# Kernel tuning notes

Hardware: AMD Instinct MI355X
Metric: run time of the kernel (lower is better)

## Reference

```python
import jax, jax.numpy as jnp
import numpy as np
from jax import lax

N, IN_CH, FEAT, OUT_CH, H, W = 8, 3, 64, 3, 256, 256
EPS = 1e-8


def lrelu(x):
    return jnp.where(x >= 0, x, 0.2 * x)


def conv2d(x, w, b, stride, pad):
    y = lax.conv_general_dilated(x, w, (stride, stride), [(pad, pad), (pad, pad)],
                                 dimension_numbers=('NCHW', 'OIHW', 'NCHW'))
    return y + b[None, :, None, None]


def make_blur_kernel():
    # _make_kernel([1,3,3,1]): outer product, normalized
    k = jnp.array([1.0, 3.0, 3.0, 1.0], jnp.float32)
    k = k[None, :] * k[:, None]
    return k / k.sum()


def blur(x, kernel, pad):
    # upfirdn2d with up=down=1: pad then FIR-convolve (true convolution -> flip kernel)
    n, c, h, w = x.shape
    k = jnp.flip(kernel, (0, 1))[None, None]  # [1,1,kh,kw]
    y = lax.conv_general_dilated(x.reshape(n * c, 1, h, w), k, (1, 1),
                                 [(pad[0], pad[1]), (pad[0], pad[1])],
                                 dimension_numbers=('NCHW', 'OIHW', 'NCHW'))
    return y.reshape(n, c, y.shape[-2], y.shape[-1])


def mod_conv(x, s, w, swW, swb, sbW, sbb, mode, blur_k, activate=True):
    # x [n,c,h,w]; s [n,feat]; w [out,c,k,k]; style 1x1 convs on [n,feat,1,1] == matmuls
    kk = w.shape[-1]
    sw = lrelu(s @ swW.T + swb)                    # [n, c]  (style_weight)
    sb = lrelu(s @ sbW.T + sbb)                    # [n, out] (style_bias)
    weight = w[None] * sw[:, None, :, None, None]  # [n,out,c,k,k]
    d = lax.rsqrt(jnp.sum(weight * weight, axis=(2, 3, 4)) + EPS)
    weight = weight * d[:, :, None, None, None]    # demodulate
    if mode == 'up':
        # conv_transpose2d(stride=2, pad=0) == conv with lhs_dilation=2, pad k-1, flipped kernel
        wf = jnp.flip(weight, (-2, -1))
        def f(xi, wi):
            return lax.conv_general_dilated(xi[None], wi, (1, 1),
                    [(kk - 1, kk - 1)] * 2, lhs_dilation=(2, 2),
                    dimension_numbers=('NCHW', 'OIHW', 'NCHW'))[0]
        y = jax.vmap(f)(x, wf)
        y = blur(y, blur_k * 4.0, (1, 1))          # Blur(pad=(1,1), upsample_factor=2)
    elif mode == 'down':
        xb = blur(x, blur_k, (2, 2))               # Blur(pad=(2,2))
        def f(xi, wi):
            return lax.conv_general_dilated(xi[None], wi, (2, 2), [(0, 0)] * 2,
                    dimension_numbers=('NCHW', 'OIHW', 'NCHW'))[0]
        y = jax.vmap(f)(xb, weight)
    else:
        p = kk // 2
        def f(xi, wi):
            return lax.conv_general_dilated(xi[None], wi, (1, 1), [(p, p)] * 2,
                    dimension_numbers=('NCHW', 'OIHW', 'NCHW'))[0]
        y = jax.vmap(f)(x, weight)
    y = y + sb[:, :, None, None]
    return lrelu(y) if activate else y


def da_forward(x, ref, g0_w, g0_b, gr_w, gr_b,
               c0_w, c0_swW, c0_swb, c0_sbW, c0_sbb,
               mid_w, mid_swW, mid_swb, mid_sbW, mid_sbb,
               c6_w, c6_swW, c6_swb, c6_sbW, c6_sbb):
    bk = make_blur_kernel()
    # guide_net: conv s1/lrelu, conv s2/lrelu, conv s1/lrelu, conv s2/lrelu, conv s1, avgpool(1)
    h = lrelu(conv2d(ref, g0_w, g0_b, 1, 1))
    strides = (2, 1, 2, 1)
    for i in range(4):
        h = conv2d(h, gr_w[i], gr_b[i], strides[i], 1)
        if i < 3:
            h = lrelu(h)
    s = jnp.mean(h, axis=(2, 3))  # [n, feat]; AdaptiveAvgPool2d(1)

    mids = lambda i: (mid_w[i], mid_swW[i], mid_swb[i], mid_sbW[i], mid_sbb[i])
    f0 = mod_conv(x, s, c0_w, c0_swW, c0_swb, c0_sbW, c0_sbb, 'none', bk)
    f1 = mod_conv(f0, s, *mids(0), 'down', bk)
    f1 = mod_conv(f1, s, *mids(1), 'none', bk)
    f2 = mod_conv(f1, s, *mids(2), 'down', bk)
    f2 = mod_conv(f2, s, *mids(3), 'none', bk)
    f3 = mod_conv(f2, s, *mids(4), 'none', bk)
    f3 = mod_conv(f3, s, *mids(5), 'none', bk)
    f4 = mod_conv(f3 + f2, s, *mids(6), 'up', bk)
    f4 = mod_conv(f4, s, *mids(7), 'none', bk)
    f5 = mod_conv(f4 + f1, s, *mids(8), 'up', bk)
    f5 = mod_conv(f5, s, *mids(9), 'none', bk)
    out = mod_conv(f5 + f0, s, c6_w, c6_swW, c6_swb, c6_sbW, c6_sbb, 'none', bk, activate=False)
    return out


def setup_inputs() -> dict:
    key = jax.random.key(0)
    ks = jax.random.split(key, 24)
    f = FEAT
    inv = 1.0 / np.sqrt(f)
    d = {
        'x':   jax.random.normal(ks[0], (N, IN_CH, H, W), jnp.float32),
        'ref': jax.random.normal(ks[1], (N, IN_CH, H, W), jnp.float32),
        'g0_w': jax.random.normal(ks[2], (f, IN_CH, 3, 3), jnp.float32) * (1.0 / np.sqrt(IN_CH * 9)),
        'g0_b': jnp.zeros((f,), jnp.float32),
        'gr_w': jax.random.normal(ks[3], (4, f, f, 3, 3), jnp.float32) * (1.0 / np.sqrt(f * 9)),
        'gr_b': jnp.zeros((4, f), jnp.float32),
        'c0_w':   jax.random.normal(ks[4], (f, IN_CH, 3, 3), jnp.float32),
        'c0_swW': jax.random.normal(ks[5], (IN_CH, f), jnp.float32) * inv,
        'c0_swb': jnp.zeros((IN_CH,), jnp.float32),
        'c0_sbW': jax.random.normal(ks[6], (f, f), jnp.float32) * inv,
        'c0_sbb': jnp.zeros((f,), jnp.float32),
        'mid_w':   jax.random.normal(ks[7], (10, f, f, 3, 3), jnp.float32),
        'mid_swW': jax.random.normal(ks[8], (10, f, f), jnp.float32) * inv,
        'mid_swb': jnp.zeros((10, f), jnp.float32),
        'mid_sbW': jax.random.normal(ks[9], (10, f, f), jnp.float32) * inv,
        'mid_sbb': jnp.zeros((10, f), jnp.float32),
        'c6_w':   jax.random.normal(ks[10], (OUT_CH, f, 3, 3), jnp.float32),
        'c6_swW': jax.random.normal(ks[11], (f, f), jnp.float32) * inv,
        'c6_swb': jnp.zeros((f,), jnp.float32),
        'c6_sbW': jax.random.normal(ks[12], (OUT_CH, f), jnp.float32) * inv,
        'c6_sbb': jnp.zeros((OUT_CH,), jnp.float32),
    }
    return d


def reference(x, ref, g0_w, g0_b, gr_w, gr_b,
              c0_w, c0_swW, c0_swb, c0_sbW, c0_sbb,
              mid_w, mid_swW, mid_swb, mid_sbW, mid_sbb,
              c6_w, c6_swW, c6_swb, c6_sbW, c6_sbb):
    return da_forward(x, ref, g0_w, g0_b, gr_w, gr_b,
                      c0_w, c0_swW, c0_swb, c0_sbW, c0_sbb,
                      mid_w, mid_swW, mid_swb, mid_sbW, mid_sbb,
                      c6_w, c6_swW, c6_swb, c6_sbW, c6_sbb)
```

## Files before the change

### kernel.cpp

```cpp
#include <hip/hip_runtime.h>

#define LRELU(v) ((v) >= 0.f ? (v) : 0.2f * (v))

template<int S>
__global__ void conv64_gemm(const float* __restrict__ in, const float* __restrict__ Wt,
                            const float* __restrict__ bias, float* __restrict__ out,
                            int Hin, int Win, int Hout, int Wout, int pad, int act, int tilesX,
                            long long inStr, long long wStr, long long bStr, long long outStr)
{
    constexpr int CC  = (S == 1) ? 8 : 4;
    constexpr int TIN = (S == 1) ? 18 : 33;
    constexpr int RS  = (S == 1) ? 20 : 36;
    constexpr int NF4 = (S == 1) ? 3 : 5;
    constexpr int PW  = NF4 * 4;
    extern __shared__ float lds[];
    float* it = lds;
    float* wl = lds + CC * TIN * RS;

    int s = blockIdx.y;
    in   += (size_t)s * inStr;
    Wt   += (size_t)s * wStr;
    bias += (size_t)s * bStr;
    out  += (size_t)s * outStr;

    int b  = blockIdx.x;
    int tx = b % tilesX, ty = b / tilesX;
    int t  = threadIdx.x;
    int og = t >> 5;
    int pg = t & 31;
    int r  = pg >> 1, ch = pg & 1;

    float acc[8][8];
    #pragma unroll
    for (int i = 0; i < 8; ++i)
        #pragma unroll
        for (int j = 0; j < 8; ++j) acc[i][j] = 0.f;

    const int y0 = ty * 16 * S - pad;
    const int x0 = tx * 16 * S - pad;
    const size_t plane = (size_t)Hin * Win;

    for (int c0 = 0; c0 < 64; c0 += CC) {
        __syncthreads();
        {
            const float4* src = (const float4*)(Wt + c0 * 9 * 64);
            float4* dst = (float4*)wl;
            for (int i = t; i < CC * 9 * 16; i += 256) dst[i] = src[i];
        }
        for (int rowi = t; rowi < CC * TIN; rowi += 256) {
            int cc = rowi / TIN, rr = rowi - cc * TIN;
            int iy = y0 + rr;
            float* dst = it + (size_t)rowi * RS;
            const float* srow = in + (size_t)(c0 + cc) * plane + (size_t)iy * Win + x0;
            if ((unsigned)iy < (unsigned)Hin && x0 >= 0 && x0 + RS <= Win) {
                #pragma unroll
                for (int q = 0; q < RS / 4; ++q)
                    ((float4*)dst)[q] = ((const float4*)srow)[q];
            } else {
                for (int cl = 0; cl < TIN; ++cl) {
                    int ix = x0 + cl;
                    float v = 0.f;
                    if ((unsigned)iy < (unsigned)Hin && (unsigned)ix < (unsigned)Win)
                        v = in[(size_t)(c0 + cc) * plane + (size_t)iy * Win + ix];
                    dst[cl] = v;
                }
            }
        }
        __syncthreads();
        for (int cc = 0; cc < CC; ++cc) {
            const float* base = it + cc * TIN * RS;
            #pragma unroll
            for (int ky = 0; ky < 3; ++ky) {
                float p[PW];
                const float* rowp = base + (r * S + ky) * RS + ch * 8 * S;
                #pragma unroll
                for (int q = 0; q < NF4; ++q) {
                    float4 f = *(const float4*)(rowp + q * 4);
                    p[q*4+0] = f.x; p[q*4+1] = f.y; p[q*4+2] = f.z; p[q*4+3] = f.w;
                }
                #pragma unroll
                for (int kx = 0; kx < 3; ++kx) {
                    const float* wp = wl + ((cc * 9) + ky * 3 + kx) * 64 + og * 8;
                    float4 wa = *(const float4*)wp;
                    float4 wb = *(const float4*)(wp + 4);
                    float w8[8] = {wa.x, wa.y, wa.z, wa.w, wb.x, wb.y, wb.z, wb.w};
                    #pragma unroll
                    for (int oi = 0; oi < 8; ++oi)
                        #pragma unroll
                        for (int j = 0; j < 8; ++j)
                            acc[oi][j] += w8[oi] * p[j * S + kx];
                }
            }
        }
    }

    int y  = ty * 16 + r;
    int xb = tx * 16 + ch * 8;
    #pragma unroll
    for (int oi = 0; oi < 8; ++oi) {
        int o = og * 8 + oi;
        float bo = bias[o];
        float v[8];
        #pragma unroll
        for (int j = 0; j < 8; ++j) {
            float a = acc[oi][j] + bo;
            v[j] = act ? LRELU(a) : a;
        }
        float* op = out + ((size_t)o * Hout + y) * Wout + xb;
        *(float4*)op       = make_float4(v[0], v[1], v[2], v[3]);
        *(float4*)(op + 4) = make_float4(v[4], v[5], v[6], v[7]);
    }
}

__global__ void conv64_gemm8(const float* __restrict__ in, const float* __restrict__ Wt,
                             const float* __restrict__ bias, float* __restrict__ out,
                             int H, int W, int act, int tilesX,
                             long long inStr, long long wStr, long long bStr, long long outStr)
{
    constexpr int CC = 8, TIN = 10, RS = 12;
    __shared__ float it[CC * TIN * RS];
    __shared__ float wl[CC * 9 * 64];
    int s = blockIdx.y;
    in   += (size_t)s * inStr;
    Wt   += (size_t)s * wStr;
    bias += (size_t)s * bStr;
    out  += (size_t)s * outStr;

    int b  = blockIdx.x;
    int tx = b % tilesX, ty = b / tilesX;
    int t  = threadIdx.x;
    int og = t >> 5, pg = t & 31;
    int r  = pg >> 2, ch = pg & 3;

    float acc[8][2];
    #pragma unroll
    for (int i = 0; i < 8; ++i) { acc[i][0] = 0.f; acc[i][1] = 0.f; }

    const int y0 = ty * 8 - 1, x0 = tx * 8 - 1;
    const size_t plane = (size_t)H * W;

    for (int c0 = 0; c0 < 64; c0 += CC) {
        __syncthreads();
        {
            const float4* src = (const float4*)(Wt + c0 * 9 * 64);
            float4* dst = (float4*)wl;
            for (int i = t; i < CC * 9 * 16; i += 256) dst[i] = src[i];
        }
        for (int rowi = t; rowi < CC * TIN; rowi += 256) {
            int cc = rowi / TIN, rr = rowi - cc * TIN;
            int iy = y0 + rr;
            float* dst = it + rowi * RS;
            const float* srow = in + (size_t)(c0 + cc) * plane + (size_t)iy * W + x0;
            if ((unsigned)iy < (unsigned)H && x0 >= 0 && x0 + RS <= W) {
                #pragma unroll
                for (int q = 0; q < 3; ++q)
                    ((float4*)dst)[q] = ((const float4*)srow)[q];
            } else {
                for (int cl = 0; cl < RS; ++cl) {
                    int ix = x0 + cl;
                    float v = 0.f;
                    if (cl < TIN && (unsigned)iy < (unsigned)H && (unsigned)ix < (unsigned)W)
                        v = in[(size_t)(c0 + cc) * plane + (size_t)iy * W + ix];
                    dst[cl] = v;
                }
            }
        }
        __syncthreads();
        for (int cc = 0; cc < CC; ++cc) {
            const float* base = it + cc * TIN * RS;
            #pragma unroll
            for (int ky = 0; ky < 3; ++ky) {
                const float* rowp = base + (r + ky) * RS + ch * 2;
                float p[4] = {rowp[0], rowp[1], rowp[2], rowp[3]};
                #pragma unroll
                for (int kx = 0; kx < 3; ++kx) {
                    const float* wp = wl + ((cc * 9) + ky * 3 + kx) * 64 + og * 8;
                    float4 wa = *(const float4*)wp;
                    float4 wb = *(const float4*)(wp + 4);
                    float w8[8] = {wa.x, wa.y, wa.z, wa.w, wb.x, wb.y, wb.z, wb.w};
                    #pragma unroll
                    for (int oi = 0; oi < 8; ++oi) {
                        acc[oi][0] += w8[oi] * p[kx];
                        acc[oi][1] += w8[oi] * p[kx + 1];
                    }
                }
            }
        }
    }

    int y = ty * 8 + r, xb = tx * 8 + ch * 2;
    #pragma unroll
    for (int oi = 0; oi < 8; ++oi) {
        int o = og * 8 + oi;
        float bo = bias[o];
        float a0 = acc[oi][0] + bo, a1 = acc[oi][1] + bo;
        if (act) { a0 = LRELU(a0); a1 = LRELU(a1); }
        *(float2*)(out + ((size_t)o * H + y) * W + xb) = make_float2(a0, a1);
    }
}

__global__ void conv3_gemm(const float* __restrict__ in, const float* __restrict__ Wt,
                           const float* __restrict__ bias, float* __restrict__ out,
                           int H, int W, int tilesX,
                           long long inStr, long long wStr, long long bStr, long long outStr)
{
    constexpr int TIN = 18, RS = 20;
    __shared__ float it[3 * TIN * RS];
    __shared__ float wl[27 * 64];
    int s = blockIdx.y;
    in   += (size_t)s * inStr;
    Wt   += (size_t)s * wStr;
    bias += (size_t)s * bStr;
    out  += (size_t)s * outStr;

    int b  = blockIdx.x;
    int tx = b % tilesX, ty = b / tilesX;
    int t  = threadIdx.x;
    {
        const float4* src = (const float4*)Wt;
        float4* dst = (float4*)wl;
        for (int i = t; i < 27 * 16; i += 256) dst[i] = src[i];
    }
    const int y0 = ty * 16 - 1, x0 = tx * 16 - 1;
    const size_t plane = (size_t)H * W;
    for (int rowi = t; rowi < 3 * TIN; rowi += 256) {
        int cc = rowi / TIN, rr = rowi - cc * TIN;
        int iy = y0 + rr;
        float* dst = it + (size_t)rowi * RS;
        const float* srow = in + (size_t)cc * plane + (size_t)iy * W + x0;
        if ((unsigned)iy < (unsigned)H && x0 >= 0 && x0 + RS <= W) {
            #pragma unroll
            for (int q = 0; q < RS / 4; ++q)
                ((float4*)dst)[q] = ((const float4*)srow)[q];
        } else {
            for (int cl = 0; cl < TIN; ++cl) {
                int ix = x0 + cl;
                float v = 0.f;
                if ((unsigned)iy < (unsigned)H && (unsigned)ix < (unsigned)W)
                    v = in[(size_t)cc * plane + (size_t)iy * W + ix];
                dst[cl] = v;
            }
        }
    }
    __syncthreads();

    int og = t >> 5, pg = t & 31;
    int r  = pg >> 1, ch = pg & 1;
    float acc[8][8];
    #pragma unroll
    for (int i = 0; i < 8; ++i)
        #pragma unroll
        for (int j = 0; j < 8; ++j) acc[i][j] = 0.f;

    for (int c = 0; c < 3; ++c) {
        const float* base = it + c * TIN * RS;
        #pragma unroll
        for (int ky = 0; ky < 3; ++ky) {
            float p[12];
            const float* rowp = base + (r + ky) * RS + ch * 8;
            #pragma unroll
            for (int q = 0; q < 3; ++q) {
                float4 f = *(const float4*)(rowp + q * 4);
                p[q*4+0] = f.x; p[q*4+1] = f.y; p[q*4+2] = f.z; p[q*4+3] = f.w;
            }
            #pragma unroll
            for (int kx = 0; kx < 3; ++kx) {
                const float* wp = wl + ((c * 9) + ky * 3 + kx) * 64 + og * 8;
                float4 wa = *(const float4*)wp;
                float4 wb = *(const float4*)(wp + 4);
                float w8[8] = {wa.x, wa.y, wa.z, wa.w, wb.x, wb.y, wb.z, wb.w};
                #pragma unroll
                for (int oi = 0; oi < 8; ++oi)
                    #pragma unroll
                    for (int j = 0; j < 8; ++j)
                        acc[oi][j] += w8[oi] * p[j + kx];
            }
        }
    }

    int y  = ty * 16 + r;
    int xb = tx * 16 + ch * 8;
    #pragma unroll
    for (int oi = 0; oi < 8; ++oi) {
        int o = og * 8 + oi;
        float bo = bias[o];
        float v[8];
        #pragma unroll
        for (int j = 0; j < 8; ++j) {
            float a = acc[oi][j] + bo;
            v[j] = LRELU(a);
        }
        float* op = out + ((size_t)o * H + y) * W + xb;
        *(float4*)op       = make_float4(v[0], v[1], v[2], v[3]);
        *(float4*)(op + 4) = make_float4(v[4], v[5], v[6], v[7]);
    }
}

__global__ void conv64to3_gemm(const float* __restrict__ in, const float* __restrict__ in2,
                               const float* __restrict__ Wt, const float* __restrict__ sb,
                               float* __restrict__ out, int H, int W, int tilesX,
                               long long inStr, long long wStr, long long sbStr, long long outStr)
{
    constexpr int CC = 8, TIN = 18, RS = 20;
    __shared__ float it[CC * TIN * RS];
    __shared__ float wl[CC * 9 * 3];
    int s = blockIdx.y;
    in  += (size_t)s * inStr;
    in2 += (size_t)s * inStr;
    Wt  += (size_t)s * wStr;
    sb  += (size_t)s * sbStr;
    out += (size_t)s * outStr;

    int b  = blockIdx.x;
    int tx = b % tilesX, ty = b / tilesX;
    int t  = threadIdx.x;
    int r  = t >> 4, cl = t & 15;
    const int y0 = ty * 16 - 1, x0 = tx * 16 - 1;
    const size_t plane = (size_t)H * W;

    float acc[3] = {0.f, 0.f, 0.f};

    for (int c0 = 0; c0 < 64; c0 += CC) {
        __syncthreads();
        for (int i = t; i < CC * 9 * 3; i += 256) wl[i] = Wt[c0 * 27 + i];
        for (int rowi = t; rowi < CC * TIN; rowi += 256) {
            int cc = rowi / TIN, rr = rowi - cc * TIN;
            int iy = y0 + rr;
            float* dst = it + (size_t)rowi * RS;
            size_t roff = (size_t)(c0 + cc) * plane + (size_t)iy * W + x0;
            if ((unsigned)iy < (unsigned)H && x0 >= 0 && x0 + RS <= W) {
                #pragma unroll
                for (int q = 0; q < RS / 4; ++q) {
                    float4 a = ((const float4*)(in  + roff))[q];
                    float4 bb = ((const float4*)(in2 + roff))[q];
                    ((float4*)dst)[q] = make_float4(a.x + bb.x, a.y + bb.y, a.z + bb.z, a.w + bb.w);
                }
            } else {
                for (int c2 = 0; c2 < TIN; ++c2) {
                    int ix = x0 + c2;
                    float v = 0.f;
                    if ((unsigned)iy < (unsigned)H && (unsigned)ix < (unsigned)W) {
                        size_t off = (size_t)(c0 + cc) * plane + (size_t)iy * W + ix;
                        v = in[off] + in2[off];
                    }
                    dst[c2] = v;
                }
            }
        }
        __syncthreads();
        for (int cc = 0; cc < CC; ++cc) {
            const float* base = it + cc * TIN * RS;
            #pragma unroll
            for (int ky = 0; ky < 3; ++ky) {
                const float* rowp = base + (r + ky) * RS + cl;
                float p0 = rowp[0], p1 = rowp[1], p2 = rowp[2];
                const float* wr = wl + (cc * 9 + ky * 3) * 3;
                #pragma unroll
                for (int o = 0; o < 3; ++o)
                    acc[o] += wr[o] * p0 + wr[3 + o] * p1 + wr[6 + o] * p2;
            }
        }
    }

    int y = ty * 16 + r, x = tx * 16 + cl;
    #pragma unroll
    for (int o = 0; o < 3; ++o)
        out[((size_t)o * H + y) * W + x] = acc[o] + sb[o];
}

__global__ void upconv64_gemm(const float* __restrict__ in, const float* __restrict__ in2,
                              const float* __restrict__ G2, const float* __restrict__ sb,
                              float* __restrict__ out, int Hin, int Win, int tilesX,
                              long long bufStr, long long sbStr, long long outStr)
{
    constexpr int CC = 4;
    constexpr int RS = 12;
    constexpr int PSTR = 68;
    extern __shared__ float lds[];
    float* it = lds;
    float* wl = lds + CC * 10 * RS;

    int s = blockIdx.y;
    in  += (size_t)s * bufStr;
    in2 += (size_t)s * bufStr;
    G2  += (size_t)s * bufStr;
    sb  += (size_t)s * sbStr;
    out += (size_t)s * outStr;

    int b  = blockIdx.x;
    int tx = b % tilesX, ty = b / tilesX;
    int t  = threadIdx.x;
    int og    = t & 7;
    int pxb   = (t >> 3) & 1;
    int rhalf = (t >> 4) & 7;
    int rpar  = t >> 7;
    int r = 2 * rhalf + rpar;
    const int Y0 = ty * 16, X0 = tx * 16;
    const int gy0 = Y0 / 2 - 1;
    const int gx0 = X0 / 2 - 1;
    const size_t plane = (size_t)Hin * Win;

    float acc[8][8];
    #pragma unroll
    for (int i = 0; i < 8; ++i)
        #pragma unroll
        for (int j = 0; j < 8; ++j) acc[i][j] = 0.f;

    for (int c0 = 0; c0 < 64; c0 += CC) {
        __syncthreads();
        {
            const float4* src = (const float4*)(G2 + (size_t)c0 * 2304);
            for (int i = t; i < CC * 36 * 16; i += 256) {
                int row = i >> 4, q = i & 15;
                ((float4*)(wl + row * PSTR))[q] = src[i];
            }
        }
        for (int rowi = t; rowi < CC * 10; rowi += 256) {
            int cc = rowi / 10, rr = rowi - cc * 10;
            int gi = gy0 + rr;
            float* dst = it + (size_t)rowi * RS;
            size_t roff = (size_t)(c0 + cc) * plane + (size_t)gi * Win + gx0;
            if ((unsigned)gi < (unsigned)Hin && gx0 >= 0 && gx0 + RS <= Win) {
                #pragma unroll
                for (int qq = 0; qq < 3; ++qq) {
                    float4 a = ((const float4*)(in  + roff))[qq];
                    float4 bb = ((const float4*)(in2 + roff))[qq];
                    ((float4*)dst)[qq] = make_float4(a.x + bb.x, a.y + bb.y, a.z + bb.z, a.w + bb.w);
                }
            } else {
                for (int cl = 0; cl < RS; ++cl) {
                    int gj = gx0 + cl;
                    float v = 0.f;
                    if (cl < 10 && (unsigned)gi < (unsigned)Hin && (unsigned)gj < (unsigned)Win) {
                        size_t off = (size_t)(c0 + cc) * plane + (size_t)gi * Win + gj;
                        v = in[off] + in2[off];
                    }
                    dst[cl] = v;
                }
            }
        }
        __syncthreads();
        for (int cc = 0; cc < CC; ++cc) {
            const float* ib = it + cc * 10 * RS;
            const float* wcb = wl + cc * (36 * PSTR) + (rpar * 2 + pxb) * PSTR;
            #pragma unroll
            for (int ty2 = 0; ty2 < 3; ++ty2) {
                float p[12];
                const float* rowp = ib + (rhalf + ty2) * RS;
                #pragma unroll
                for (int qq = 0; qq < 3; ++qq) {
                    float4 f = *(const float4*)(rowp + qq * 4);
                    p[qq*4+0] = f.x; p[qq*4+1] = f.y; p[qq*4+2] = f.z; p[qq*4+3] = f.w;
                }
                #pragma unroll
                for (int tx2 = 0; tx2 < 3; ++tx2) {
                    const float* wp = wcb + (ty2 * 3 + tx2) * (4 * PSTR) + og * 8;
                    float4 wa = *(const float4*)wp;
                    float4 wv = *(const float4*)(wp + 4);
                    float w8[8] = {wa.x, wa.y, wa.z, wa.w, wv.x, wv.y, wv.z, wv.w};
                    #pragma unroll
                    for (int oi = 0; oi < 8; ++oi)
                        #pragma unroll
                        for (int k = 0; k < 8; ++k)
                            acc[oi][k] += w8[oi] * p[k + tx2];
                }
            }
        }
    }

    const int Hout = 2 * Hin, Wout = 2 * Win;
    int y = Y0 + r;
    #pragma unroll
    for (int oi = 0; oi < 8; ++oi) {
        int o = og * 8 + oi;
        float bo = sb[o];
        float v[8];
        #pragma unroll
        for (int k = 0; k < 8; ++k) {
            float a = acc[oi][k] + bo;
            v[k] = LRELU(a);
        }
        float rcv[4];
        #pragma unroll
        for (int j = 0; j < 4; ++j) {
            float snd = pxb ? v[j] : v[4 + j];
            rcv[j] = __shfl_xor(snd, 8, 64);
        }
        float w0 = pxb ? rcv[0] : v[0];
        float w1 = pxb ? v[4]   : rcv[0];
        float w2 = pxb ? rcv[1] : v[1];
        float w3 = pxb ? v[5]   : rcv[1];
        float w4 = pxb ? rcv[2] : v[2];
        float w5 = pxb ? v[6]   : rcv[2];
        float w6 = pxb ? rcv[3] : v[3];
        float w7 = pxb ? v[7]   : rcv[3];
        float* op = out + ((size_t)o * Hout + y) * Wout + X0 + (pxb ? 8 : 0);
        *(float4*)op       = make_float4(w0, w1, w2, w3);
        *(float4*)(op + 4) = make_float4(w4, w5, w6, w7);
    }
}

__global__ void combine_up_w(const float* __restrict__ W, float* __restrict__ G2,
                             long long wStr, long long g2Str)
{
    int s = blockIdx.y;
    W  += (size_t)s * wStr;
    G2 += (size_t)s * g2Str;
    int i = blockIdx.x * 256 + threadIdx.x;
    if (i >= 147456) return;
    int o = i & 63;
    int rest = i >> 6;
    int p4 = rest & 3;
    int k9 = (rest >> 2) % 9;
    int c  = (rest >> 2) / 9;
    int py = p4 >> 1, px = p4 & 1;
    int tyk = k9 / 3, txk = k9 % 3;
    int dy = 2 * tyk - 1 - py, dx = 2 * txk - 1 - px;
    const float K[4] = {1.f, 3.f, 3.f, 1.f};
    const float* wp = W + ((size_t)o * 64 + c) * 9;
    float sacc = 0.f;
    #pragma unroll
    for (int a = 0; a < 3; ++a) {
        int ky = a + dy;
        if ((unsigned)ky >= 4u) continue;
        #pragma unroll
        for (int b2 = 0; b2 < 3; ++b2) {
            int kx = b2 + dx;
            if ((unsigned)kx >= 4u) continue;
            sacc += K[ky] * K[kx] * wp[a * 3 + b2];
        }
    }
    G2[i] = sacc * (1.f / 16.f);
}

__global__ void blur_down(const float* __restrict__ in, float* __restrict__ out,
                          int H, int W, int tilesX, int tilesY,
                          long long inStr, long long outStr)
{
    int s = blockIdx.y;
    in  += (size_t)s * inStr;
    out += (size_t)s * outStr;
    int Ho = H + 1, Wo = W + 1;
    int bid = blockIdx.x;
    int tx = bid % tilesX; bid /= tilesX;
    int ty = bid % tilesY; bid /= tilesY;
    int p  = bid;
    int x = tx * 16 + (threadIdx.x & 15);
    int y = ty * 16 + (threadIdx.x >> 4);
    if (x >= Wo || y >= Ho) return;
    const float k[4] = {1.f, 3.f, 3.f, 1.f};
    const float* ip = in + (size_t)p * H * W;
    float acc = 0.f;
    #pragma unroll
    for (int ky = 0; ky < 4; ++ky) {
        int iy = y - 2 + ky;
        if ((unsigned)iy >= (unsigned)H) continue;
        float row = 0.f;
        #pragma unroll
        for (int kx = 0; kx < 4; ++kx) {
            int ix = x - 2 + kx;
            if ((unsigned)ix >= (unsigned)W) continue;
            row += ip[(size_t)iy * W + ix] * k[kx];
        }
        acc += row * k[ky];
    }
    out[((size_t)p * Ho + y) * Wo + x] = acc * (1.f / 64.f);
}

__global__ void avgpool_hw(const float* __restrict__ in, float* __restrict__ out, int HW,
                           long long inStr, long long outStr)
{
    int s = blockIdx.y;
    in  += (size_t)s * inStr;
    out += (size_t)s * outStr;
    int p = blockIdx.x;
    const float* ip = in + (size_t)p * HW;
    float sum = 0.f;
    for (int i = threadIdx.x; i < HW; i += blockDim.x) sum += ip[i];
    __shared__ float red[256];
    red[threadIdx.x] = sum;
    __syncthreads();
    for (int off = 128; off; off >>= 1) {
        if ((int)threadIdx.x < off) red[threadIdx.x] += red[threadIdx.x + off];
        __syncthreads();
    }
    if (threadIdx.x == 0) out[p] = red[0] / (float)HW;
}

__global__ void style_fc(const float* __restrict__ s, const float* __restrict__ W,
                         const float* __restrict__ b, float* __restrict__ out, int outdim)
{
    int n = blockIdx.x;
    int i = threadIdx.x;
    if (i >= outdim) return;
    float acc = b[i];
    const float* sn = s + n * 64;
    const float* wi = W + i * 64;
    for (int f = 0; f < 64; ++f) acc += sn[f] * wi[f];
    out[n * 64 + i] = LRELU(acc);
}

__global__ void modulate(const float* __restrict__ w, const float* __restrict__ sw,
                         float* __restrict__ wout, int O, int C, int transpose)
{
    int no = blockIdx.x;
    int o = no % O, n = no / O;
    int nw = C * 9;
    int t = threadIdx.x;
    float v[9];
    int cnt = 0;
    float ss = 0.f;
    for (int idx = t; idx < nw; idx += 64) {
        int c = idx / 9;
        float val = w[o * nw + idx] * sw[n * 64 + c];
        v[cnt++] = val;
        ss += val * val;
    }
    #pragma unroll
    for (int off = 32; off; off >>= 1) ss += __shfl_xor(ss, off);
    float d = rsqrtf(ss + 1e-8f);
    cnt = 0;
    for (int idx = t; idx < nw; idx += 64) {
        float val = v[cnt++] * d;
        if (transpose)
            wout[(size_t)n * nw * O + (size_t)idx * O + o] = val;
        else
            wout[(size_t)no * nw + idx] = val;
    }
}

__global__ void guide_transpose(const float* __restrict__ grw, float* __restrict__ gt, int total)
{
    int i = blockIdx.x * 256 + threadIdx.x;
    if (i >= total) return;
    int l = i / 36864, rem = i % 36864;
    int idx = rem / 64, o = rem % 64;
    int c = idx / 9, k = idx % 9;
    gt[i] = grw[(((size_t)l * 64 + o) * 64 + c) * 9 + k];
}

__global__ void g0_transpose(const float* __restrict__ g0w, float* __restrict__ gt)
{
    int i = blockIdx.x * 256 + threadIdx.x;
    if (i >= 1728) return;
    int idx = i / 64, o = i % 64;
    int c = idx / 9, k = idx % 9;
    gt[i] = g0w[((size_t)o * 3 + c) * 9 + k];
}

__global__ void fill_sentinel(float* __restrict__ out, int n)
{
    int i = blockIdx.x * 256 + threadIdx.x;
    if (i < n) out[i] = 1.0e9f;
}

extern "C" void kernel_launch(void* const* d_in, const int* in_sizes, int n_in,
                              void* d_out, int out_size, void* d_ws, size_t ws_size,
                              hipStream_t stream)
{
    const float* x     = (const float*)d_in[0];
    const float* ref   = (const float*)d_in[1];
    const float* g0w   = (const float*)d_in[2];
    const float* g0b   = (const float*)d_in[3];
    const float* grw   = (const float*)d_in[4];
    const float* grb   = (const float*)d_in[5];
    const float* c0w   = (const float*)d_in[6];
    const float* c0swW = (const float*)d_in[7];
    const float* c0swb = (const float*)d_in[8];
    const float* c0sbW = (const float*)d_in[9];
    const float* c0sbb = (const float*)d_in[10];
    const float* midw  = (const float*)d_in[11];
    const float* midswW= (const float*)d_in[12];
    const float* midswb= (const float*)d_in[13];
    const float* midsbW= (const float*)d_in[14];
    const float* midsbb= (const float*)d_in[15];
    const float* c6w   = (const float*)d_in[16];
    const float* c6swW = (const float*)d_in[17];
    const float* c6swb = (const float*)d_in[18];
    const float* c6sbW = (const float*)d_in[19];
    const float* c6sbb = (const float*)d_in[20];
    float* out = (float*)d_out;
    float* ws  = (float*)d_ws;

    const size_t SV  = 0;
    const size_t STY = 512;
    const size_t WM  = 12800;
    const size_t GT  = 2989568;
    const size_t G0T = 3137024;
    const size_t BUF = 3138816;

    const size_t SA = 0;
    const size_t SB = 4227136;
    const size_t D1 = 8421440;
    const size_t D2 = 9470016;
    const size_t D3 = 10518592;
    const size_t E1 = 11583616;
    const size_t E2 = 11845760;
    const size_t E3 = 12107904;
    const size_t G2o = 12370048;
    const long long PER = 12517504ll;

    const size_t gSA = 0;
    const size_t gD1 = 4194304;
    const size_t gD2 = 5242880;
    const size_t gE1 = 6291456;
    const size_t gE2 = 6553600;
    const long long GPER = 6815744ll;

    int G = 0, GG = 0;
    for (int g = 8; g >= 1; --g)
        if ((BUF + (size_t)g * PER) * sizeof(float) <= ws_size) { G = g; break; }
    for (int g = 8; g >= 1; --g)
        if ((BUF + (size_t)g * GPER) * sizeof(float) <= ws_size) { GG = g; break; }
    if (!G || !GG) {
        fill_sentinel<<<dim3((out_size + 255) / 256), dim3(256), 0, stream>>>(out, out_size);
        return;
    }

    dim3 blk(256);
    const int LDS1 = 29952;
    const int LDS2 = 28224;
    const int LDSU = (4 * 10 * 12 + 4 * 2448) * 4;

    float* B = ws + BUF;

    guide_transpose<<<dim3(147456 / 256), blk, 0, stream>>>(grw, ws + GT, 147456);
    g0_transpose<<<dim3(7), blk, 0, stream>>>(g0w, ws + G0T);

    for (int n0 = 0; n0 < 8; ) {
        int g = (8 - n0 < GG) ? (8 - n0) : GG;
        const float* refg = ref + (size_t)n0 * 196608;
        conv3_gemm<<<dim3(16 * 16, g), blk, 0, stream>>>(
            refg, ws + G0T, g0b, B + gSA, 256, 256, 16, 196608, 0, 0, GPER);
        conv64_gemm<2><<<dim3(8 * 8, g), blk, LDS2, stream>>>(
            B + gSA, ws + GT, grb, B + gD1, 256, 256, 128, 128, 1, 1, 8, GPER, 0, 0, GPER);
        conv64_gemm<1><<<dim3(8 * 8, g), blk, LDS1, stream>>>(
            B + gD1, ws + GT + 36864, grb + 64, B + gD2, 128, 128, 128, 128, 1, 1, 8, GPER, 0, 0, GPER);
        conv64_gemm<2><<<dim3(4 * 4, g), blk, LDS2, stream>>>(
            B + gD2, ws + GT + 73728, grb + 128, B + gE1, 128, 128, 64, 64, 1, 1, 4, GPER, 0, 0, GPER);
        conv64_gemm8<<<dim3(8 * 8, g), blk, 0, stream>>>(
            B + gE1, ws + GT + 110592, grb + 192, B + gE2, 64, 64, 0, 8, GPER, 0, 0, GPER);
        avgpool_hw<<<dim3(64, g), blk, 0, stream>>>(B + gE2, ws + SV + (size_t)n0 * 64, 4096, GPER, 64);
        n0 += g;
    }

    const float* Wt[12];  const float* swWp[12]; const float* swbp[12];
    const float* sbWp[12]; const float* sbbp[12];
    int Ci[12], Oi[12];
    size_t wmo[12];
    Wt[0] = c0w; swWp[0] = c0swW; swbp[0] = c0swb; sbWp[0] = c0sbW; sbbp[0] = c0sbb;
    Ci[0] = 3; Oi[0] = 64; wmo[0] = WM;
    for (int i = 0; i < 10; ++i) {
        Wt[1 + i]   = midw   + (size_t)i * 36864;
        swWp[1 + i] = midswW + (size_t)i * 4096;
        swbp[1 + i] = midswb + (size_t)i * 64;
        sbWp[1 + i] = midsbW + (size_t)i * 4096;
        sbbp[1 + i] = midsbb + (size_t)i * 64;
        Ci[1 + i] = 64; Oi[1 + i] = 64;
        wmo[1 + i] = WM + 13824ull + (size_t)i * 294912ull;
    }
    Wt[11] = c6w; swWp[11] = c6swW; swbp[11] = c6swb; sbWp[11] = c6sbW; sbbp[11] = c6sbb;
    Ci[11] = 64; Oi[11] = 3; wmo[11] = WM + 13824ull + 2949120ull;

    const int trf[12] = {1, 1, 1, 1, 1, 1, 1, 0, 1, 0, 1, 1};

    for (int i = 0; i < 12; ++i) {
        style_fc<<<dim3(8), dim3(64), 0, stream>>>(ws + SV, swWp[i], swbp[i], ws + STY + i * 1024, Ci[i]);
        style_fc<<<dim3(8), dim3(64), 0, stream>>>(ws + SV, sbWp[i], sbbp[i], ws + STY + i * 1024 + 512, Oi[i]);
        modulate<<<dim3(8 * Oi[i]), dim3(64), 0, stream>>>(Wt[i], ws + STY + i * 1024, ws + wmo[i], Oi[i], Ci[i], trf[i]);
    }

    for (int n0 = 0; n0 < 8; ) {
        int g = (8 - n0 < G) ? (8 - n0) : G;
        const float* xg = x + (size_t)n0 * 196608;
        float* outg = out + (size_t)n0 * 196608;
        #define WN(i)  (ws + wmo[i] + (size_t)n0 * Oi[i] * Ci[i] * 9)
        #define WSTR(i) ((long long)(Oi[i] * Ci[i] * 9))
        #define SBN(i) (ws + STY + (i) * 1024 + 512 + (size_t)n0 * 64)
        conv3_gemm<<<dim3(16 * 16, g), blk, 0, stream>>>(
            xg, WN(0), SBN(0), B + SB, 256, 256, 16, 196608, WSTR(0), 64, PER);
        blur_down<<<dim3(64 * 17 * 17, g), blk, 0, stream>>>(B + SB, B + SA, 256, 256, 17, 17, PER, PER);
        conv64_gemm<2><<<dim3(8 * 8, g), blk, LDS2, stream>>>(
            B + SA, WN(1), SBN(1), B + D1, 257, 257, 128, 128, 0, 1, 8, PER, WSTR(1), 64, PER);
        conv64_gemm8<<<dim3(16 * 16, g), blk, 0, stream>>>(
            B + D1, WN(2), SBN(2), B + D2, 128, 128, 1, 16, PER, WSTR(2), 64, PER);
        blur_down<<<dim3(64 * 9 * 9, g), blk, 0, stream>>>(B + D2, B + D3, 128, 128, 9, 9, PER, PER);
        conv64_gemm<2><<<dim3(4 * 4, g), blk, LDS2, stream>>>(
            B + D3, WN(3), SBN(3), B + E1, 129, 129, 64, 64, 0, 1, 4, PER, WSTR(3), 64, PER);
        conv64_gemm8<<<dim3(8 * 8, g), blk, 0, stream>>>(
            B + E1, WN(4), SBN(4), B + E2, 64, 64, 1, 8, PER, WSTR(4), 64, PER);
        conv64_gemm8<<<dim3(8 * 8, g), blk, 0, stream>>>(
            B + E2, WN(5), SBN(5), B + E3, 64, 64, 1, 8, PER, WSTR(5), 64, PER);
        conv64_gemm8<<<dim3(8 * 8, g), blk, 0, stream>>>(
            B + E3, WN(6), SBN(6), B + E1, 64, 64, 1, 8, PER, WSTR(6), 64, PER);
        combine_up_w<<<dim3(576, g), blk, 0, stream>>>(WN(7), B + G2o, WSTR(7), PER);
        upconv64_gemm<<<dim3(8 * 8, g), blk, LDSU, stream>>>(
            B + E1, B + E2, B + G2o, SBN(7), B + D1, 64, 64, 8, PER, 64, PER);
        conv64_gemm8<<<dim3(16 * 16, g), blk, 0, stream>>>(
            B + D1, WN(8), SBN(8), B + D3, 128, 128, 1, 16, PER, WSTR(8), 64, PER);
        combine_up_w<<<dim3(576, g), blk, 0, stream>>>(WN(9), B + G2o, WSTR(9), PER);
        upconv64_gemm<<<dim3(16 * 16, g), blk, LDSU, stream>>>(
            B + D3, B + D2, B + G2o, SBN(9), B + SA, 128, 128, 16, PER, 64, PER);
        conv64_gemm<1><<<dim3(16 * 16, g), blk, LDS1, stream>>>(
            B + SA, WN(10), SBN(10), B + SB, 256, 256, 256, 256, 1, 1, 16, PER, WSTR(10), 64, PER);
        conv3_gemm<<<dim3(16 * 16, g), blk, 0, stream>>>(
            xg, WN(0), SBN(0), B + SA, 256, 256, 16, 196608, WSTR(0), 64, PER);
        conv64to3_gemm<<<dim3(16 * 16, g), blk, 0, stream>>>(
            B + SB, B + SA, WN(11), SBN(11), outg, 256, 256, 16, PER, WSTR(11), 64, 196608);
        #undef WN
        #undef WSTR
        #undef SBN
        n0 += g;
    }
}
```

Before: 4.600 ms.

## Add small-tile stride-2 conv kernel and retile upconv for more blocks

```diff
diff --git a/kernel.cpp b/kernel.cpp
--- a/kernel.cpp
+++ b/kernel.cpp
@@ -196,6 +196,95 @@
         float a0 = acc[oi][0] + bo, a1 = acc[oi][1] + bo;
         if (act) { a0 = LRELU(a0); a1 = LRELU(a1); }
         *(float2*)(out + ((size_t)o * H + y) * W + xb) = make_float2(a0, a1);
+    }
+}
+
+__global__ void conv64s2_gemm8(const float* __restrict__ in, const float* __restrict__ Wt,
+                               const float* __restrict__ bias, float* __restrict__ out,
+                               int Hin, int Win, int Hout, int Wout, int pad, int act, int tilesX,
+                               long long inStr, long long wStr, long long bStr, long long outStr)
+{
+    constexpr int CC = 8, TIN = 18, RS = 20;
+    __shared__ float it[CC * TIN * RS];
+    __shared__ float wl[CC * 9 * 64];
+    int s = blockIdx.y;
+    in   += (size_t)s * inStr;
+    Wt   += (size_t)s * wStr;
+    bias += (size_t)s * bStr;
+    out  += (size_t)s * outStr;
+
+    int b  = blockIdx.x;
+    int tx = b % tilesX, ty = b / tilesX;
+    int t  = threadIdx.x;
+    int og = t >> 5, pg = t & 31;
+    int r  = pg >> 2, ch = pg & 3;
+
+    float acc[8][2];
+    #pragma unroll
+    for (int i = 0; i < 8; ++i) { acc[i][0] = 0.f; acc[i][1] = 0.f; }
+
+    const int y0 = ty * 16 - pad, x0 = tx * 16 - pad;
+    const size_t plane = (size_t)Hin * Win;
+
+    for (int c0 = 0; c0 < 64; c0 += CC) {
+        __syncthreads();
+        {
+            const float4* src = (const float4*)(Wt + c0 * 9 * 64);
+            float4* dst = (float4*)wl;
+            for (int i = t; i < CC * 9 * 16; i += 256) dst[i] = src[i];
+        }
+        for (int rowi = t; rowi < CC * TIN; rowi += 256) {
+            int cc = rowi / TIN, rr = rowi - cc * TIN;
+            int iy = y0 + rr;
+            float* dst = it + rowi * RS;
+            const float* srow = in + (size_t)(c0 + cc) * plane + (size_t)iy * Win + x0;
+            if ((unsigned)iy < (unsigned)Hin && x0 >= 0 && x0 + RS <= Win) {
+                #pragma unroll
+                for (int q = 0; q < RS / 4; ++q)
+                    ((float4*)dst)[q] = ((const float4*)srow)[q];
+            } else {
+                for (int cl = 0; cl < RS; ++cl) {
+                    int ix = x0 + cl;
+                    float v = 0.f;
+                    if (cl < TIN && (unsigned)iy < (unsigned)Hin && (unsigned)ix < (unsigned)Win)
+                        v = in[(size_t)(c0 + cc) * plane + (size_t)iy * Win + ix];
+                    dst[cl] = v;
+                }
+            }
+        }
+        __syncthreads();
+        for (int cc = 0; cc < CC; ++cc) {
+            const float* base = it + cc * TIN * RS;
+            #pragma unroll
+            for (int ky = 0; ky < 3; ++ky) {
+                const float* rowp = base + (2 * r + ky) * RS + ch * 4;
+                float4 f0 = *(const float4*)rowp;
+                float4 f1 = *(const float4*)(rowp + 4);
+                float p[8] = {f0.x, f0.y, f0.z, f0.w, f1.x, f1.y, f1.z, f1.w};
+                #pragma unroll
+                for (int kx = 0; kx < 3; ++kx) {
+                    const float* wp = wl + ((cc * 9) + ky * 3 + kx) * 64 + og * 8;
+                    float4 wa = *(const float4*)wp;
+                    float4 wb = *(const float4*)(wp + 4);
+                    float w8[8] = {wa.x, wa.y, wa.z, wa.w, wb.x, wb.y, wb.z, wb.w};
+                    #pragma unroll
+                    for (int oi = 0; oi < 8; ++oi) {
+                        acc[oi][0] += w8[oi] * p[kx];
+                        acc[oi][1] += w8[oi] * p[kx + 2];
+                    }
+                }
+            }
+        }
+    }
+
+    int y = ty * 8 + r, xb = tx * 8 + ch * 2;
+    #pragma unroll
+    for (int oi = 0; oi < 8; ++oi) {
+        int o = og * 8 + oi;
+        float bo = bias[o];
+        float a0 = acc[oi][0] + bo, a1 = acc[oi][1] + bo;
+        if (act) { a0 = LRELU(a0); a1 = LRELU(a1); }
+        *(float2*)(out + ((size_t)o * Hout + y) * Wout + xb) = make_float2(a0, a1);
     }
 }
 
@@ -374,11 +463,11 @@
                               long long bufStr, long long sbStr, long long outStr)
 {
     constexpr int CC = 4;
-    constexpr int RS = 12;
+    constexpr int RS = 20;
     constexpr int PSTR = 68;
     extern __shared__ float lds[];
     float* it = lds;
-    float* wl = lds + CC * 10 * RS;
+    float* wl = lds + CC * 6 * RS;
 
     int s = blockIdx.y;
     in  += (size_t)s * bufStr;
@@ -390,12 +479,12 @@
     int b  = blockIdx.x;
     int tx = b % tilesX, ty = b / tilesX;
     int t  = threadIdx.x;
-    int og    = t & 7;
-    int pxb   = (t >> 3) & 1;
-    int rhalf = (t >> 4) & 7;
-    int rpar  = t >> 7;
-    int r = 2 * rhalf + rpar;
-    const int Y0 = ty * 16, X0 = tx * 16;
+    int og  = t & 7;
+    int pxb = (t >> 3) & 1;
+    int xh  = (t >> 4) & 1;
+    int r   = t >> 5;
+    int rhalf = r >> 1, rpar = r & 1;
+    const int Y0 = ty * 8, X0 = tx * 32;
     const int gy0 = Y0 / 2 - 1;
     const int gx0 = X0 / 2 - 1;
     const size_t plane = (size_t)Hin * Win;
@@ -415,14 +504,14 @@
                 ((float4*)(wl + row * PSTR))[q] = src[i];
             }
         }
-        for (int rowi = t; rowi < CC * 10; rowi += 256) {
-            int cc = rowi / 10, rr = rowi - cc * 10;
+        for (int rowi = t; rowi < CC * 6; rowi += 256) {
+            int cc = rowi / 6, rr = rowi - cc * 6;
             int gi = gy0 + rr;
             float* dst = it + (size_t)rowi * RS;
             size_t roff = (size_t)(c0 + cc) * plane + (size_t)gi * Win + gx0;
             if ((unsigned)gi < (unsigned)Hin && gx0 >= 0 && gx0 + RS <= Win) {
                 #pragma unroll
-                for (int qq = 0; qq < 3; ++qq) {
+                for (int qq = 0; qq < 5; ++qq) {
                     float4 a = ((const float4*)(in  + roff))[qq];
                     float4 bb = ((const float4*)(in2 + roff))[qq];
                     ((float4*)dst)[qq] = make_float4(a.x + bb.x, a.y + bb.y, a.z + bb.z, a.w + bb.w);
@@ -431,7 +520,7 @@
                 for (int cl = 0; cl < RS; ++cl) {
                     int gj = gx0 + cl;
                     float v = 0.f;
-                    if (cl < 10 && (unsigned)gi < (unsigned)Hin && (unsigned)gj < (unsigned)Win) {
+                    if (cl < 18 && (unsigned)gi < (unsigned)Hin && (unsigned)gj < (unsigned)Win) {
                         size_t off = (size_t)(c0 + cc) * plane + (size_t)gi * Win + gj;
                         v = in[off] + in2[off];
                     }
@@ -441,12 +530,12 @@
         }
         __syncthreads();
         for (int cc = 0; cc < CC; ++cc) {
-            const float* ib = it + cc * 10 * RS;
+            const float* ib = it + cc * 6 * RS;
             const float* wcb = wl + cc * (36 * PSTR) + (rpar * 2 + pxb) * PSTR;
             #pragma unroll
             for (int ty2 = 0; ty2 < 3; ++ty2) {
                 float p[12];
-                const float* rowp = ib + (rhalf + ty2) * RS;
+                const float* rowp = ib + (rhalf + ty2) * RS + xh * 8;
                 #pragma unroll
                 for (int qq = 0; qq < 3; ++qq) {
                     float4 f = *(const float4*)(rowp + qq * 4);
@@ -494,7 +583,7 @@
         float w5 = pxb ? v[6]   : rcv[2];
         float w6 = pxb ? rcv[3] : v[3];
         float w7 = pxb ? v[7]   : rcv[3];
-        float* op = out + ((size_t)o * Hout + y) * Wout + X0 + (pxb ? 8 : 0);
+        float* op = out + ((size_t)o * Hout + y) * Wout + X0 + xh * 16 + (pxb ? 8 : 0);
         *(float4*)op       = make_float4(w0, w1, w2, w3);
         *(float4*)(op + 4) = make_float4(w4, w5, w6, w7);
     }
@@ -719,8 +808,7 @@
 
     dim3 blk(256);
     const int LDS1 = 29952;
-    const int LDS2 = 28224;
-    const int LDSU = (4 * 10 * 12 + 4 * 2448) * 4;
+    const int LDSU = (4 * 6 * 20 + 4 * 2448) * 4;
 
     float* B = ws + BUF;
 
@@ -732,12 +820,12 @@
         const float* refg = ref + (size_t)n0 * 196608;
         conv3_gemm<<<dim3(16 * 16, g), blk, 0, stream>>>(
             refg, ws + G0T, g0b, B + gSA, 256, 256, 16, 196608, 0, 0, GPER);
-        conv64_gemm<2><<<dim3(8 * 8, g), blk, LDS2, stream>>>(
-            B + gSA, ws + GT, grb, B + gD1, 256, 256, 128, 128, 1, 1, 8, GPER, 0, 0, GPER);
-        conv64_gemm<1><<<dim3(8 * 8, g), blk, LDS1, stream>>>(
-            B + gD1, ws + GT + 36864, grb + 64, B + gD2, 128, 128, 128, 128, 1, 1, 8, GPER, 0, 0, GPER);
-        conv64_gemm<2><<<dim3(4 * 4, g), blk, LDS2, stream>>>(
-            B + gD2, ws + GT + 73728, grb + 128, B + gE1, 128, 128, 64, 64, 1, 1, 4, GPER, 0, 0, GPER);
+        conv64s2_gemm8<<<dim3(16 * 16, g), blk, 0, stream>>>(
+            B + gSA, ws + GT, grb, B + gD1, 256, 256, 128, 128, 1, 1, 16, GPER, 0, 0, GPER);
+        conv64_gemm8<<<dim3(16 * 16, g), blk, 0, stream>>>(
+            B + gD1, ws + GT + 36864, grb + 64, B + gD2, 128, 128, 1, 16, GPER, 0, 0, GPER);
+        conv64s2_gemm8<<<dim3(8 * 8, g), blk, 0, stream>>>(
+            B + gD2, ws + GT + 73728, grb + 128, B + gE1, 128, 128, 64, 64, 1, 1, 8, GPER, 0, 0, GPER);
         conv64_gemm8<<<dim3(8 * 8, g), blk, 0, stream>>>(
             B + gE1, ws + GT + 110592, grb + 192, B + gE2, 64, 64, 0, 8, GPER, 0, 0, GPER);
         avgpool_hw<<<dim3(64, g), blk, 0, stream>>>(B + gE2, ws + SV + (size_t)n0 * 64, 4096, GPER, 64);
@@ -780,13 +868,13 @@
         conv3_gemm<<<dim3(16 * 16, g), blk, 0, stream>>>(
             xg, WN(0), SBN(0), B + SB, 256, 256, 16, 196608, WSTR(0), 64, PER);
         blur_down<<<dim3(64 * 17 * 17, g), blk, 0, stream>>>(B + SB, B + SA, 256, 256, 17, 17, PER, PER);
-        conv64_gemm<2><<<dim3(8 * 8, g), blk, LDS2, stream>>>(
-            B + SA, WN(1), SBN(1), B + D1, 257, 257, 128, 128, 0, 1, 8, PER, WSTR(1), 64, PER);
+        conv64s2_gemm8<<<dim3(16 * 16, g), blk, 0, stream>>>(
+            B + SA, WN(1), SBN(1), B + D1, 257, 257, 128, 128, 0, 1, 16, PER, WSTR(1), 64, PER);
         conv64_gemm8<<<dim3(16 * 16, g), blk, 0, stream>>>(
             B + D1, WN(2), SBN(2), B + D2, 128, 128, 1, 16, PER, WSTR(2), 64, PER);
         blur_down<<<dim3(64 * 9 * 9, g), blk, 0, stream>>>(B + D2, B + D3, 128, 128, 9, 9, PER, PER);
-        conv64_gemm<2><<<dim3(4 * 4, g), blk, LDS2, stream>>>(
-            B + D3, WN(3), SBN(3), B + E1, 129, 129, 64, 64, 0, 1, 4, PER, WSTR(3), 64, PER);
+        conv64s2_gemm8<<<dim3(8 * 8, g), blk, 0, stream>>>(
+            B + D3, WN(3), SBN(3), B + E1, 129, 129, 64, 64, 0, 1, 8, PER, WSTR(3), 64, PER);
         conv64_gemm8<<<dim3(8 * 8, g), blk, 0, stream>>>(
             B + E1, WN(4), SBN(4), B + E2, 64, 64, 1, 8, PER, WSTR(4), 64, PER);
         conv64_gemm8<<<dim3(8 * 8, g), blk, 0, stream>>>(
@@ -794,13 +882,13 @@
         conv64_gemm8<<<dim3(8 * 8, g), blk, 0, stream>>>(
             B + E3, WN(6), SBN(6), B + E1, 64, 64, 1, 8, PER, WSTR(6), 64, PER);
         combine_up_w<<<dim3(576, g), blk, 0, stream>>>(WN(7), B + G2o, WSTR(7), PER);
-        upconv64_gemm<<<dim3(8 * 8, g), blk, LDSU, stream>>>(
-            B + E1, B + E2, B + G2o, SBN(7), B + D1, 64, 64, 8, PER, 64, PER);
+        upconv64_gemm<<<dim3(4 * 16, g), blk, LDSU, stream>>>(
+            B + E1, B + E2, B + G2o, SBN(7), B + D1, 64, 64, 4, PER, 64, PER);
         conv64_gemm8<<<dim3(16 * 16, g), blk, 0, stream>>>(
             B + D1, WN(8), SBN(8), B + D3, 128, 128, 1, 16, PER, WSTR(8), 64, PER);
         combine_up_w<<<dim3(576, g), blk, 0, stream>>>(WN(9), B + G2o, WSTR(9), PER);
-        upconv64_gemm<<<dim3(16 * 16, g), blk, LDSU, stream>>>(
-            B + D3, B + D2, B + G2o, SBN(9), B + SA, 128, 128, 16, PER, 64, PER);
+        upconv64_gemm<<<dim3(8 * 32, g), blk, LDSU, stream>>>(
+            B + D3, B + D2, B + G2o, SBN(9), B + SA, 128, 128, 8, PER, 64, PER);
         conv64_gemm<1><<<dim3(16 * 16, g), blk, LDS1, stream>>>(
             B + SA, WN(10), SBN(10), B + SB, 256, 256, 256, 256, 1, 1, 16, PER, WSTR(10), 64, PER);
         conv3_gemm<<<dim3(16 * 16, g), blk, 0, stream>>>(
```

After: 4.302 ms. -6.5%, faster.
